# Kernel tuning notes

Hardware: AMD Instinct MI355X
Metric: run time of the kernel (lower is better)

Reference implementation:

```python
import jax, jax.numpy as jnp
import numpy as np

N = 2_000_000


def skew(w):
    # (...,3) -> (...,3,3)
    x, y, z = w[..., 0], w[..., 1], w[..., 2]
    o = jnp.zeros_like(x)
    return jnp.stack([jnp.stack([o, -z, y], -1),
                      jnp.stack([z, o, -x], -1),
                      jnp.stack([-y, x, o], -1)], -2)


def srodrigues(xi, q):
    # Screw exponential (Rodrigues): xi = (w, v) 6-vector, q: (N,) joint values -> (N,4,4)
    w, v = xi[:3], xi[3:]
    th = jnp.linalg.norm(w)
    safe = jnp.maximum(th, 1e-12)
    wn, vn = w / safe, v / safe
    phi = q * th                                   # (N,)
    W = skew(wn)
    W2 = W @ W
    s = jnp.sin(phi)[:, None, None]
    c = (1.0 - jnp.cos(phi))[:, None, None]
    I3 = jnp.eye(3, dtype=q.dtype)
    R = I3 + s * W + c * W2                        # (N,3,3)
    G = phi[:, None, None] * I3 + c * W + (phi[:, None, None] - s) * W2
    p = jnp.einsum('nij,j->ni', G, vn)             # (N,3)
    rot = th > 1e-9                                # pure-translation fallback
    R = jnp.where(rot, R, jnp.broadcast_to(I3, R.shape))
    p = jnp.where(rot, p, q[:, None] * v)
    n = q.shape[0]
    bottom = jnp.broadcast_to(jnp.array([0., 0., 0., 1.], q.dtype), (n, 1, 4))
    return jnp.concatenate([jnp.concatenate([R, p[..., None]], -1), bottom], -2)


def body_twist(T, xi):
    # Ad_{T^-1} = [[R^T, 0], [-R^T [p]x, R^T]]
    R = T[..., :3, :3]
    p = T[..., :3, 3]
    w, v = xi[:3], xi[3:]
    Rt = jnp.swapaxes(R, -1, -2)
    wb = jnp.einsum('nij,j->ni', Rt, w)
    vb = jnp.einsum('nij,nj->ni', Rt, v - jnp.cross(p, jnp.broadcast_to(w, p.shape)))
    return jnp.concatenate([wb, vb], -1)           # (N,6)


def _random_se3(key, n):
    k1, k2 = jax.random.split(key)
    a = jax.random.normal(k1, (n, 3))
    th = jnp.linalg.norm(a, axis=-1, keepdims=True)  # (n,1)
    wn = a / (th + 1e-9)
    W = skew(wn)
    W2 = W @ W
    s = jnp.sin(th)[..., None]
    c = (1.0 - jnp.cos(th))[..., None]
    R = jnp.eye(3, dtype=jnp.float32) + s * W + c * W2
    p = jax.random.normal(k2, (n, 3))
    bottom = jnp.broadcast_to(jnp.array([0., 0., 0., 1.], jnp.float32), (n, 1, 4))
    return jnp.concatenate([jnp.concatenate([R, p[..., None]], -1), bottom], -2)


def setup_inputs() -> dict:
    key = jax.random.key(0)
    k1, k2, k3, k4 = jax.random.split(key, 4)
    out = _random_se3(k1, N)                                       # (N,4,4) valid SE(3)
    q_single_value = jax.random.normal(k2, (N, 2), dtype=jnp.float32)
    revolute = jax.random.uniform(k3, (6,), minval=-1.0, maxval=1.0, dtype=jnp.float32)
    prismatic = jax.random.uniform(k4, (6,), minval=-1.0, maxval=1.0, dtype=jnp.float32)
    return {'out': out, 'q_single_value': q_single_value,
            'revolute': revolute, 'prismatic': prismatic}


def reference(out, q_single_value, revolute, prismatic):
    revoluteTwist = body_twist(out, revolute)                       # (N,6)
    out = jnp.einsum('nij,njk->nik', out, srodrigues(revolute, q_single_value[:, 0]))
    prismaticTwist = body_twist(out, prismatic)                     # (N,6)
    out = jnp.einsum('nij,njk->nik', out, srodrigues(prismatic, q_single_value[:, 1]))
    return (revoluteTwist, prismaticTwist, out)
```

## Files before the change

### kernel.cpp

```cpp
#include <hip/hip_runtime.h>


__device__ __forceinline__ void body_twist6(
    const float4& r0, const float4& r1, const float4& r2,
    float wx, float wy, float wz, float vx, float vy, float vz,
    float t[6])
{
    const float px = r0.w, py = r1.w, pz = r2.w;
    const float ux = vx - (py * wz - pz * wy);
    const float uy = vy - (pz * wx - px * wz);
    const float uz = vz - (px * wy - py * wx);
    t[0] = r0.x * wx + r1.x * wy + r2.x * wz;
    t[1] = r0.y * wx + r1.y * wy + r2.y * wz;
    t[2] = r0.z * wx + r1.z * wy + r2.z * wz;
    t[3] = r0.x * ux + r1.x * uy + r2.x * uz;
    t[4] = r0.y * ux + r1.y * uy + r2.y * uz;
    t[5] = r0.z * ux + r1.z * uy + r2.z * uz;
}

__device__ __forceinline__ void apply_srodrigues(
    float4& r0, float4& r1, float4& r2,
    float th, bool rot,
    float wnx, float wny, float wnz,
    float vnx, float vny, float vnz,
    float vx, float vy, float vz,
    float q)
{
    float R00, R01, R02, R10, R11, R12, R20, R21, R22, p0, p1, p2;
    if (rot) {
        const float phi = q * th;
        float s, cv;
        sincosf(phi, &s, &cv);
        const float c = 1.0f - cv;
        R00 = 1.0f + c * (wnx * wnx - 1.0f);
        R01 = -s * wnz + c * wnx * wny;
        R02 =  s * wny + c * wnx * wnz;
        R10 =  s * wnz + c * wny * wnx;
        R11 = 1.0f + c * (wny * wny - 1.0f);
        R12 = -s * wnx + c * wny * wnz;
        R20 = -s * wny + c * wnz * wnx;
        R21 =  s * wnx + c * wnz * wny;
        R22 = 1.0f + c * (wnz * wnz - 1.0f);
        const float d  = wnx * vnx + wny * vny + wnz * vnz;
        const float cx = wny * vnz - wnz * vny;
        const float cy = wnz * vnx - wnx * vnz;
        const float cz = wnx * vny - wny * vnx;
        const float ps = phi - s;
        p0 = phi * vnx + c * cx + ps * (wnx * d - vnx);
        p1 = phi * vny + c * cy + ps * (wny * d - vny);
        p2 = phi * vnz + c * cz + ps * (wnz * d - vnz);
    } else {
        R00 = 1.0f; R01 = 0.0f; R02 = 0.0f;
        R10 = 0.0f; R11 = 1.0f; R12 = 0.0f;
        R20 = 0.0f; R21 = 0.0f; R22 = 1.0f;
        p0 = q * vx; p1 = q * vy; p2 = q * vz;
    }
    float4 n0, n1, n2;
    n0.x = r0.x * R00 + r0.y * R10 + r0.z * R20;
    n0.y = r0.x * R01 + r0.y * R11 + r0.z * R21;
    n0.z = r0.x * R02 + r0.y * R12 + r0.z * R22;
    n0.w = r0.x * p0  + r0.y * p1  + r0.z * p2 + r0.w;
    n1.x = r1.x * R00 + r1.y * R10 + r1.z * R20;
    n1.y = r1.x * R01 + r1.y * R11 + r1.z * R21;
    n1.z = r1.x * R02 + r1.y * R12 + r1.z * R22;
    n1.w = r1.x * p0  + r1.y * p1  + r1.z * p2 + r1.w;
    n2.x = r2.x * R00 + r2.y * R10 + r2.z * R20;
    n2.y = r2.x * R01 + r2.y * R11 + r2.z * R21;
    n2.z = r2.x * R02 + r2.y * R12 + r2.z * R22;
    n2.w = r2.x * p0  + r2.y * p1  + r2.z * p2 + r2.w;
    r0 = n0; r1 = n1; r2 = n2;
}

__global__ __launch_bounds__(256) void twist_66322884985439_kernel(
    const float* __restrict__ Tin,
    const float* __restrict__ q2,
    const float* __restrict__ rev,
    const float* __restrict__ pri,
    float* __restrict__ outRev,
    float* __restrict__ outPri,
    float* __restrict__ outT,
    int n)
{
    const int i = blockIdx.x * blockDim.x + threadIdx.x;
    if (i >= n) return;

    const float rwx = rev[0], rwy = rev[1], rwz = rev[2];
    const float rvx = rev[3], rvy = rev[4], rvz = rev[5];
    const float pwx = pri[0], pwy = pri[1], pwz = pri[2];
    const float pvx = pri[3], pvy = pri[4], pvz = pri[5];

    const float rth  = sqrtf(rwx * rwx + rwy * rwy + rwz * rwz);
    const float rinv = 1.0f / fmaxf(rth, 1e-12f);
    const bool  rrot = rth > 1e-9f;
    const float rwnx = rwx * rinv, rwny = rwy * rinv, rwnz = rwz * rinv;
    const float rvnx = rvx * rinv, rvny = rvy * rinv, rvnz = rvz * rinv;

    const float pth  = sqrtf(pwx * pwx + pwy * pwy + pwz * pwz);
    const float pinv = 1.0f / fmaxf(pth, 1e-12f);
    const bool  prot = pth > 1e-9f;
    const float pwnx = pwx * pinv, pwny = pwy * pinv, pwnz = pwz * pinv;
    const float pvnx = pvx * pinv, pvny = pvy * pinv, pvnz = pvz * pinv;

    const float4* Tp = reinterpret_cast<const float4*>(Tin + (size_t)i * 16);
    float4 r0 = Tp[0];
    float4 r1 = Tp[1];
    float4 r2 = Tp[2];

    const float2 q = *reinterpret_cast<const float2*>(q2 + (size_t)i * 2);

    float tr[6];
    body_twist6(r0, r1, r2, rwx, rwy, rwz, rvx, rvy, rvz, tr);

    apply_srodrigues(r0, r1, r2, rth, rrot, rwnx, rwny, rwnz, rvnx, rvny, rvnz,
                     rvx, rvy, rvz, q.x);

    float tp[6];
    body_twist6(r0, r1, r2, pwx, pwy, pwz, pvx, pvy, pvz, tp);

    apply_srodrigues(r0, r1, r2, pth, prot, pwnx, pwny, pwnz, pvnx, pvny, pvnz,
                     pvx, pvy, pvz, q.y);

    float2* orv = reinterpret_cast<float2*>(outRev + (size_t)i * 6);
    orv[0] = make_float2(tr[0], tr[1]);
    orv[1] = make_float2(tr[2], tr[3]);
    orv[2] = make_float2(tr[4], tr[5]);

    float2* opv = reinterpret_cast<float2*>(outPri + (size_t)i * 6);
    opv[0] = make_float2(tp[0], tp[1]);
    opv[1] = make_float2(tp[2], tp[3]);
    opv[2] = make_float2(tp[4], tp[5]);

    float4* ot = reinterpret_cast<float4*>(outT + (size_t)i * 16);
    ot[0] = r0;
    ot[1] = r1;
    ot[2] = r2;
    ot[3] = make_float4(0.0f, 0.0f, 0.0f, 1.0f);
}

extern "C" void kernel_launch(void* const* d_in, const int* in_sizes, int n_in,
                              void* d_out, int out_size, void* d_ws, size_t ws_size,
                              hipStream_t stream) {
    const float* Tin = (const float*)d_in[0];
    const float* q2  = (const float*)d_in[1];
    const float* rev = (const float*)d_in[2];
    const float* pri = (const float*)d_in[3];

    const int n = in_sizes[0] / 16;

    float* out = (float*)d_out;
    float* outRev = out;
    float* outPri = out + (size_t)n * 6;
    float* outT   = out + (size_t)n * 12;

    const int block = 256;
    const int grid = (n + block - 1) / block;
    twist_66322884985439_kernel<<<grid, block, 0, stream>>>(
        Tin, q2, rev, pri, outRev, outPri, outT, n);
}
```

Before: 333.6 us.

## Stage twist outputs in LDS for coalesced stores, use nontemporal access and fast sincos

Per-thread twist results are written to shared memory, then copied out by the block as contiguous float4 nontemporal stores instead of strided float2 stores. Input loads and transform stores become nontemporal. The full-precision sincosf is replaced with the __sinf/__cosf intrinsics. This adds a block barrier and LDS traffic, and lowers the accuracy of sin/cos for large arguments.

```diff
diff --git a/kernel.cpp b/kernel.cpp
--- a/kernel.cpp
+++ b/kernel.cpp
@@ -1,8 +1,13 @@
 #include <hip/hip_runtime.h>
 
 
+#define BLOCK 256
+
+typedef float vf4 __attribute__((ext_vector_type(4)));
+typedef float vf2 __attribute__((ext_vector_type(2)));
+
 __device__ __forceinline__ void body_twist6(
-    const float4& r0, const float4& r1, const float4& r2,
+    const vf4& r0, const vf4& r1, const vf4& r2,
     float wx, float wy, float wz, float vx, float vy, float vz,
     float t[6])
 {
@@ -19,7 +24,7 @@
 }
 
 __device__ __forceinline__ void apply_srodrigues(
-    float4& r0, float4& r1, float4& r2,
+    vf4& r0, vf4& r1, vf4& r2,
     float th, bool rot,
     float wnx, float wny, float wnz,
     float vnx, float vny, float vnz,
@@ -29,9 +34,9 @@
     float R00, R01, R02, R10, R11, R12, R20, R21, R22, p0, p1, p2;
     if (rot) {
         const float phi = q * th;
-        float s, cv;
-        sincosf(phi, &s, &cv);
-        const float c = 1.0f - cv;
+        const float s  = __sinf(phi);
+        const float cv = __cosf(phi);
+        const float c  = 1.0f - cv;
         R00 = 1.0f + c * (wnx * wnx - 1.0f);
         R01 = -s * wnz + c * wnx * wny;
         R02 =  s * wny + c * wnx * wnz;
@@ -55,7 +60,7 @@
         R20 = 0.0f; R21 = 0.0f; R22 = 1.0f;
         p0 = q * vx; p1 = q * vy; p2 = q * vz;
     }
-    float4 n0, n1, n2;
+    vf4 n0, n1, n2;
     n0.x = r0.x * R00 + r0.y * R10 + r0.z * R20;
     n0.y = r0.x * R01 + r0.y * R11 + r0.z * R21;
     n0.z = r0.x * R02 + r0.y * R12 + r0.z * R22;
@@ -71,7 +76,7 @@
     r0 = n0; r1 = n1; r2 = n2;
 }
 
-__global__ __launch_bounds__(256) void twist_66322884985439_kernel(
+__global__ __launch_bounds__(BLOCK) void twist_66322884985439_kernel(
     const float* __restrict__ Tin,
     const float* __restrict__ q2,
     const float* __restrict__ rev,
@@ -81,8 +86,14 @@
     float* __restrict__ outT,
     int n)
 {
-    const int i = blockIdx.x * blockDim.x + threadIdx.x;
-    if (i >= n) return;
+    __shared__ float sRev[BLOCK * 6];
+    __shared__ float sPri[BLOCK * 6];
+
+    const int tid = threadIdx.x;
+    const int blockStart = blockIdx.x * BLOCK;
+    const int i = blockStart + tid;
+    const bool active = i < n;
+    const int li = active ? i : (n - 1);
 
     const float rwx = rev[0], rwy = rev[1], rwz = rev[2];
     const float rvx = rev[3], rvy = rev[4], rvz = rev[5];
@@ -101,40 +112,57 @@
     const float pwnx = pwx * pinv, pwny = pwy * pinv, pwnz = pwz * pinv;
     const float pvnx = pvx * pinv, pvny = pvy * pinv, pvnz = pvz * pinv;
 
-    const float4* Tp = reinterpret_cast<const float4*>(Tin + (size_t)i * 16);
-    float4 r0 = Tp[0];
-    float4 r1 = Tp[1];
-    float4 r2 = Tp[2];
+    const vf4* Tp = reinterpret_cast<const vf4*>(Tin + (size_t)li * 16);
+    vf4 r0 = __builtin_nontemporal_load(Tp + 0);
+    vf4 r1 = __builtin_nontemporal_load(Tp + 1);
+    vf4 r2 = __builtin_nontemporal_load(Tp + 2);
+    const vf2 q = __builtin_nontemporal_load(
+        reinterpret_cast<const vf2*>(q2 + (size_t)li * 2));
 
-    const float2 q = *reinterpret_cast<const float2*>(q2 + (size_t)i * 2);
-
-    float tr[6];
+    float tr[6], tp[6];
     body_twist6(r0, r1, r2, rwx, rwy, rwz, rvx, rvy, rvz, tr);
-
     apply_srodrigues(r0, r1, r2, rth, rrot, rwnx, rwny, rwnz, rvnx, rvny, rvnz,
                      rvx, rvy, rvz, q.x);
-
-    float tp[6];
     body_twist6(r0, r1, r2, pwx, pwy, pwz, pvx, pvy, pvz, tp);
-
     apply_srodrigues(r0, r1, r2, pth, prot, pwnx, pwny, pwnz, pvnx, pvny, pvnz,
                      pvx, pvy, pvz, q.y);
 
-    float2* orv = reinterpret_cast<float2*>(outRev + (size_t)i * 6);
-    orv[0] = make_float2(tr[0], tr[1]);
-    orv[1] = make_float2(tr[2], tr[3]);
-    orv[2] = make_float2(tr[4], tr[5]);
+    #pragma unroll
+    for (int j = 0; j < 6; ++j) sRev[tid * 6 + j] = tr[j];
+    #pragma unroll
+    for (int j = 0; j < 6; ++j) sPri[tid * 6 + j] = tp[j];
 
-    float2* opv = reinterpret_cast<float2*>(outPri + (size_t)i * 6);
-    opv[0] = make_float2(tp[0], tp[1]);
-    opv[1] = make_float2(tp[2], tp[3]);
-    opv[2] = make_float2(tp[4], tp[5]);
+    if (active) {
+        vf4* ot = reinterpret_cast<vf4*>(outT + (size_t)i * 16);
+        __builtin_nontemporal_store(r0, ot + 0);
+        __builtin_nontemporal_store(r1, ot + 1);
+        __builtin_nontemporal_store(r2, ot + 2);
+        const vf4 bottom = {0.0f, 0.0f, 0.0f, 1.0f};
+        __builtin_nontemporal_store(bottom, ot + 3);
+    }
 
-    float4* ot = reinterpret_cast<float4*>(outT + (size_t)i * 16);
-    ot[0] = r0;
-    ot[1] = r1;
-    ot[2] = r2;
-    ot[3] = make_float4(0.0f, 0.0f, 0.0f, 1.0f);
+    __syncthreads();
+
+    const int cnt  = min(BLOCK, n - blockStart);
+    const int cnt6 = cnt * 6;
+    const int nf4  = cnt6 >> 2;
+
+    {
+        const vf4* s4 = reinterpret_cast<const vf4*>(sRev);
+        vf4* g4 = reinterpret_cast<vf4*>(outRev + (size_t)blockStart * 6);
+        for (int idx = tid; idx < nf4; idx += BLOCK)
+            __builtin_nontemporal_store(s4[idx], g4 + idx);
+        for (int idx = (nf4 << 2) + tid; idx < cnt6; idx += BLOCK)
+            outRev[(size_t)blockStart * 6 + idx] = sRev[idx];
+    }
+    {
+        const vf4* s4 = reinterpret_cast<const vf4*>(sPri);
+        vf4* g4 = reinterpret_cast<vf4*>(outPri + (size_t)blockStart * 6);
+        for (int idx = tid; idx < nf4; idx += BLOCK)
+            __builtin_nontemporal_store(s4[idx], g4 + idx);
+        for (int idx = (nf4 << 2) + tid; idx < cnt6; idx += BLOCK)
+            outPri[(size_t)blockStart * 6 + idx] = sPri[idx];
+    }
 }
 
 extern "C" void kernel_launch(void* const* d_in, const int* in_sizes, int n_in,
@@ -152,8 +180,7 @@
     float* outPri = out + (size_t)n * 6;
     float* outT   = out + (size_t)n * 12;
 
-    const int block = 256;
-    const int grid = (n + block - 1) / block;
-    twist_66322884985439_kernel<<<grid, block, 0, stream>>>(
+    const int grid = (n + BLOCK - 1) / BLOCK;
+    twist_66322884985439_kernel<<<grid, BLOCK, 0, stream>>>(
         Tin, q2, rev, pri, outRev, outPri, outT, n);
 }
```

After: 410.0 us. +22.9%, slower.
